# Performance work log

Hardware: AMD Instinct MI355X
Metric: run time of the kernel (lower is better)

## Reference

```python
import jax, jax.numpy as jnp
import numpy as np

D = 1024  # model dimension

def _linear_params(key, d_in, d_out):
    kw, kb = jax.random.split(key)
    bound = 1.0 / np.sqrt(d_in)
    W = jax.random.uniform(kw, (d_out, d_in), minval=-bound, maxval=bound, dtype=jnp.float32)
    b = jax.random.uniform(kb, (d_out,), minval=-bound, maxval=bound, dtype=jnp.float32)
    return W, b

def setup_inputs() -> dict:
    key = jax.random.key(0)
    kx, ki, kq, kk, kv, ko = jax.random.split(key, 6)
    B, S = 4, 2048
    X = jax.random.normal(kx, (B, S, D), dtype=jnp.float32)
    intensity = jax.random.uniform(ki, (B, S, S), dtype=jnp.float32)
    Wq, bq = _linear_params(kq, D, D)
    Wk, bk = _linear_params(kk, D, D)
    Wv, bv = _linear_params(kv, D, D)
    Wo, bo = _linear_params(ko, D, D)
    return {"X": X, "intensity": intensity,
            "Wq": Wq, "bq": bq, "Wk": Wk, "bk": bk,
            "Wv": Wv, "bv": bv, "Wo": Wo, "bo": bo}

def reference(X, intensity, Wq, bq, Wk, bk, Wv, bv, Wo, bo):
    d_k = Wq.shape[0]
    q = X @ Wq.T + bq                      # [B,S,D]
    k = X @ Wk.T + bk                      # [B,S,D]
    v = X @ Wv.T + bv                      # [B,S,D]
    scores = jnp.einsum('bsd,btd->bst', q, k) / jnp.sqrt(jnp.asarray(d_k, X.dtype))
    attn = jax.nn.softmax(scores, axis=-1) + intensity  # non-standard additive epilogue
    out = jnp.einsum('bst,btd->bsd', attn, v)
    return out @ Wo.T + bo
```

## Files before the change

kernel.cpp:

```cpp
#include <hip/hip_runtime.h>

typedef __attribute__((ext_vector_type(8))) short bf16x8;
typedef __attribute__((ext_vector_type(4))) float f32x4;

#define LDS_TILE (48 * 1024)
#define NBUF 3
#define LDS_TOTAL (NBUF * LDS_TILE)

__device__ __forceinline__ unsigned short f2bf(float f) {
  union { float f; unsigned u; } a; a.f = f;
  unsigned u = a.u;
  unsigned r = (u + 0x7FFFu + ((u >> 16) & 1u)) >> 16;
  return (unsigned short)r;
}

__device__ __forceinline__ void stage16(const void* g, void* l) {
  __builtin_amdgcn_global_load_lds((const __attribute__((address_space(1))) unsigned int*)g,
                                   (__attribute__((address_space(3))) unsigned int*)l,
                                   16, 0, 0);
}

template<bool OUT_BF16, int BIAS_MODE>
__global__ __launch_bounds__(512) void gemm_nt(
    const unsigned short* __restrict__ A,
    const unsigned short* __restrict__ B,
    void* __restrict__ Cv,
    const float* __restrict__ bias,
    float scale, int K,
    int lda, int ldb, int ldc,
    long batchA, long batchB, long batchC)
{
  extern __shared__ char smem[];

  const int gx = gridDim.x, gy = gridDim.y;
  int bid = blockIdx.x + gx * (blockIdx.y + gy * blockIdx.z);
  const int nwg = gx * gy * gridDim.z;
  const int q = nwg >> 3;
  int wg = (bid & 7) * q + (bid >> 3);
  const int tx = wg % gx;
  int rest = wg / gx;
  const int ty = rest % gy;
  const int tz = rest / gy;

  const int tid  = threadIdx.x;
  const int lane = tid & 63;
  const int wid  = tid >> 6;
  const int wm   = wid & 3;
  const int wn   = wid >> 2;

  A += (long)tz * batchA;
  B += (long)tz * batchB;
  const int tileM = tx * 256;
  const int tileN = ty * 128;

  const int srow = tid >> 3;
  const int scol = (((tid & 7) ^ (srow & 7)) << 3);
  const unsigned short* ga[4];
  const unsigned short* gb[2];
#pragma unroll
  for (int j = 0; j < 4; ++j) ga[j] = A + (size_t)(tileM + j * 64 + srow) * lda + scol;
#pragma unroll
  for (int j = 0; j < 2; ++j) gb[j] = B + (size_t)(tileN + j * 64 + srow) * ldb + scol;

  const int frow  = lane & 15;
  const int k0slot = (lane >> 4) ^ (lane & 7);
  const int aoff = (wm * 64 + frow) * 128;
  const int boff = 32768 + (wn * 64 + frow) * 128;

  f32x4 acc[4][4];
#pragma unroll
  for (int m = 0; m < 4; ++m)
#pragma unroll
    for (int n = 0; n < 4; ++n) acc[m][n] = (f32x4){0.f, 0.f, 0.f, 0.f};

  const int nt = K >> 6;

#define STAGE(t)                                                         \
  do {                                                                   \
    char* d_ = smem + ((t) % NBUF) * LDS_TILE;                           \
    const int kc_ = (t) << 6;                                            \
    _Pragma("unroll")                                                    \
    for (int j = 0; j < 4; ++j) stage16(ga[j] + kc_, d_ + j * 8192 + tid * 16); \
    _Pragma("unroll")                                                    \
    for (int j = 0; j < 2; ++j) stage16(gb[j] + kc_, d_ + 32768 + j * 8192 + tid * 16); \
  } while (0)

#define COMPUTE(t)                                                       \
  do {                                                                   \
    const char* d_ = smem + ((t) % NBUF) * LDS_TILE;                     \
    bf16x8 af[4][2], bfr[4][2];                                          \
    _Pragma("unroll")                                                    \
    for (int ks = 0; ks < 2; ++ks) {                                     \
      const int so_ = ((k0slot ^ (ks << 2)) << 4);                       \
      _Pragma("unroll")                                                  \
      for (int m = 0; m < 4; ++m)                                        \
        af[m][ks] = *(const bf16x8*)(d_ + aoff + m * 2048 + so_);        \
      _Pragma("unroll")                                                  \
      for (int n = 0; n < 4; ++n)                                        \
        bfr[n][ks] = *(const bf16x8*)(d_ + boff + n * 2048 + so_);       \
    }                                                                    \
    __builtin_amdgcn_s_setprio(1);                                       \
    _Pragma("unroll")                                                    \
    for (int ks = 0; ks < 2; ++ks)                                       \
      _Pragma("unroll")                                                  \
      for (int m = 0; m < 4; ++m)                                        \
        _Pragma("unroll")                                                \
        for (int n = 0; n < 4; ++n)                                      \
          acc[m][n] = __builtin_amdgcn_mfma_f32_16x16x32_bf16(af[m][ks], bfr[n][ks], acc[m][n], 0, 0, 0); \
    __builtin_amdgcn_s_setprio(0);                                       \
  } while (0)

  STAGE(0);
  STAGE(1);
  asm volatile("s_waitcnt vmcnt(6)" ::: "memory");
  __builtin_amdgcn_s_barrier();

  for (int t = 0; t < nt - 2; ++t) {
    STAGE(t + 2);
    COMPUTE(t);
    asm volatile("s_waitcnt vmcnt(6)" ::: "memory");
    __builtin_amdgcn_s_barrier();
  }
  COMPUTE(nt - 2);
  asm volatile("s_waitcnt vmcnt(0)" ::: "memory");
  __builtin_amdgcn_s_barrier();
  COMPUTE(nt - 1);

#undef STAGE
#undef COMPUTE

  const int ro = (lane >> 4) << 2;
  const int co = lane & 15;
#pragma unroll
  for (int m = 0; m < 4; ++m) {
#pragma unroll
    for (int n = 0; n < 4; ++n) {
      const int row0 = tileM + wm * 64 + m * 16 + ro;
      const int col  = tileN + wn * 64 + n * 16 + co;
#pragma unroll
      for (int r = 0; r < 4; ++r) {
        float v = acc[m][n][r] * scale;
        const int row = row0 + r;
        if (BIAS_MODE == 1) v += bias[col];
        if (BIAS_MODE == 2) v += bias[row];
        const size_t ci = (size_t)(tz * batchC) + (size_t)row * ldc + col;
        if (OUT_BF16) ((unsigned short*)Cv)[ci] = f2bf(v);
        else          ((float*)Cv)[ci] = v;
      }
    }
  }
}

__global__ __launch_bounds__(256) void softmax_add_bf16(
    float* __restrict__ scores, const float* __restrict__ inten)
{
  const int row = blockIdx.x;
  float* srow = scores + (size_t)row * 2048;
  const float* irow = inten + (size_t)row * 2048;
  const int t = threadIdx.x;
  const int lane = t & 63, wid = t >> 6;

  float v[8];
  float mx = -3.4e38f;
#pragma unroll
  for (int j = 0; j < 8; ++j) { v[j] = srow[t + j * 256]; mx = fmaxf(mx, v[j]); }

  __shared__ float red[8];
#pragma unroll
  for (int o = 32; o; o >>= 1) mx = fmaxf(mx, __shfl_xor(mx, o));
  if (lane == 0) red[wid] = mx;
  __syncthreads();
  mx = fmaxf(fmaxf(red[0], red[1]), fmaxf(red[2], red[3]));

  float s = 0.f;
#pragma unroll
  for (int j = 0; j < 8; ++j) { v[j] = __expf(v[j] - mx); s += v[j]; }
#pragma unroll
  for (int o = 32; o; o >>= 1) s += __shfl_xor(s, o);
  if (lane == 0) red[4 + wid] = s;
  __syncthreads();
  s = red[4] + red[5] + red[6] + red[7];
  const float inv = 1.f / s;

  unsigned short* arow = (unsigned short*)srow;
#pragma unroll
  for (int j = 0; j < 8; ++j)
    arow[t + j * 256] = f2bf(v[j] * inv + irow[t + j * 256]);
}

__global__ __launch_bounds__(256) void cvt_bf16(
    const float* __restrict__ in, unsigned short* __restrict__ out, int n)
{
  const int i = (blockIdx.x * 256 + threadIdx.x) * 4;
  if (i >= n) return;
  const float4 f = *(const float4*)(in + i);
  ushort4 o;
  o.x = f2bf(f.x); o.y = f2bf(f.y); o.z = f2bf(f.z); o.w = f2bf(f.w);
  *(ushort4*)(out + i) = o;
}

extern "C" void kernel_launch(void* const* d_in, const int* in_sizes, int n_in,
                              void* d_out, int out_size, void* d_ws, size_t ws_size,
                              hipStream_t stream)
{
  const float* X     = (const float*)d_in[0];
  const float* inten = (const float*)d_in[1];
  const float* Wq = (const float*)d_in[2];
  const float* bq = (const float*)d_in[3];
  const float* Wk = (const float*)d_in[4];
  const float* bk = (const float*)d_in[5];
  const float* Wv = (const float*)d_in[6];
  const float* bv = (const float*)d_in[7];
  const float* Wo = (const float*)d_in[8];
  const float* bo = (const float*)d_in[9];
  float* out = (float*)d_out;

  const int B = 4, S = 2048, D = 1024;
  const int MS = B * S;
  char* ws = (char*)d_ws;
  const size_t MB = 1 << 20;
  unsigned short* Xb  = (unsigned short*)(ws);
  unsigned short* Wqb = (unsigned short*)(ws + 16 * MB);
  unsigned short* Wkb = (unsigned short*)(ws + 18 * MB);
  unsigned short* Wvb = (unsigned short*)(ws + 20 * MB);
  unsigned short* Wob = (unsigned short*)(ws + 22 * MB);
  unsigned short* Q   = (unsigned short*)(ws + 24 * MB);
  unsigned short* Kb  = (unsigned short*)(ws + 40 * MB);
  unsigned short* Vt  = (unsigned short*)(ws + 56 * MB);
  unsigned short* Oa  = (unsigned short*)(ws + 72 * MB);
  float*          Sc  = (float*)(ws + 88 * MB);

  hipFuncSetAttribute((const void*)gemm_nt<true, 1>,  hipFuncAttributeMaxDynamicSharedMemorySize, LDS_TOTAL);
  hipFuncSetAttribute((const void*)gemm_nt<true, 2>,  hipFuncAttributeMaxDynamicSharedMemorySize, LDS_TOTAL);
  hipFuncSetAttribute((const void*)gemm_nt<false, 0>, hipFuncAttributeMaxDynamicSharedMemorySize, LDS_TOTAL);
  hipFuncSetAttribute((const void*)gemm_nt<true, 0>,  hipFuncAttributeMaxDynamicSharedMemorySize, LDS_TOTAL);
  hipFuncSetAttribute((const void*)gemm_nt<false, 1>, hipFuncAttributeMaxDynamicSharedMemorySize, LDS_TOTAL);

  cvt_bf16<<<(MS * D) / 1024, 256, 0, stream>>>(X,  Xb,  MS * D);
  cvt_bf16<<<(D * D) / 1024, 256, 0, stream>>>(Wq, Wqb, D * D);
  cvt_bf16<<<(D * D) / 1024, 256, 0, stream>>>(Wk, Wkb, D * D);
  cvt_bf16<<<(D * D) / 1024, 256, 0, stream>>>(Wv, Wvb, D * D);
  cvt_bf16<<<(D * D) / 1024, 256, 0, stream>>>(Wo, Wob, D * D);

  dim3 gproj(MS / 256, D / 128, 1);
  gemm_nt<true, 1><<<gproj, 512, LDS_TOTAL, stream>>>(Xb, Wqb, Q,  bq, 1.f, D, D, D, D, 0, 0, 0);
  gemm_nt<true, 1><<<gproj, 512, LDS_TOTAL, stream>>>(Xb, Wkb, Kb, bk, 1.f, D, D, D, D, 0, 0, 0);

  dim3 gvt(D / 256, S / 128, B);
  gemm_nt<true, 2><<<gvt, 512, LDS_TOTAL, stream>>>(Wvb, Xb, Vt, bv, 1.f, D, D, D, S,
                                                    0, (long)S * D, (long)D * S);

  dim3 gsc(S / 256, S / 128, B);
  gemm_nt<false, 0><<<gsc, 512, LDS_TOTAL, stream>>>(Q, Kb, Sc, nullptr, 0.03125f, D,
                                                     D, D, S,
                                                     (long)S * D, (long)S * D, (long)S * S);

  softmax_add_bf16<<<B * S, 256, 0, stream>>>(Sc, inten);

  dim3 gav(S / 256, D / 128, B);
  gemm_nt<true, 0><<<gav, 512, LDS_TOTAL, stream>>>((unsigned short*)Sc, Vt, Oa, nullptr,
                                                    1.f, S, 2 * S, S, D,
                                                    (long)S * 2 * S, (long)D * S, (long)S * D);

  gemm_nt<false, 1><<<gproj, 512, LDS_TOTAL, stream>>>(Oa, Wob, out, bo, 1.f, D, D, D, D, 0, 0, 0);
}
```

Measured before the change: 349.8 us.

## Enlarge GEMM tiles to 256x256 with K=32 four-stage pipeline and batch Q/K projections

The GEMM kernel moves from 256x128 tiles with K-step 64 and three LDS buffers to 256x256 tiles with K-step 32 and four 32KB buffers. Each warp now computes 128x64 with 8x4 MFMA accumulators and uses a new swizzle for the narrower rows. The Q and K projections are merged into a single launch via the z dimension, with a second bias pointer picked by tz parity. The goal is more reuse per loaded byte and fewer launches, at the cost of doubled accumulator registers, a launch_bounds occupancy hint that may cause spills, and fewer workgroups per GEMM.

```diff
diff --git a/kernel.cpp b/kernel.cpp
--- a/kernel.cpp
+++ b/kernel.cpp
@@ -3,8 +3,8 @@
 typedef __attribute__((ext_vector_type(8))) short bf16x8;
 typedef __attribute__((ext_vector_type(4))) float f32x4;
 
-#define LDS_TILE (48 * 1024)
-#define NBUF 3
+#define LDS_TILE 32768
+#define NBUF 4
 #define LDS_TOTAL (NBUF * LDS_TILE)
 
 __device__ __forceinline__ unsigned short f2bf(float f) {
@@ -21,11 +21,12 @@
 }
 
 template<bool OUT_BF16, int BIAS_MODE>
-__global__ __launch_bounds__(512) void gemm_nt(
+__global__ __launch_bounds__(512, 2) void gemm_nt(
     const unsigned short* __restrict__ A,
     const unsigned short* __restrict__ B,
     void* __restrict__ Cv,
     const float* __restrict__ bias,
+    const float* __restrict__ bias2,
     float scale, int K,
     int lda, int ldb, int ldc,
     long batchA, long batchB, long batchC)
@@ -45,82 +46,80 @@
   const int tid  = threadIdx.x;
   const int lane = tid & 63;
   const int wid  = tid >> 6;
-  const int wm   = wid & 3;
-  const int wn   = wid >> 2;
+  const int wm   = wid >> 2;
+  const int wn   = wid & 3;
 
   A += (long)tz * batchA;
   B += (long)tz * batchB;
   const int tileM = tx * 256;
-  const int tileN = ty * 128;
-
-  const int srow = tid >> 3;
-  const int scol = (((tid & 7) ^ (srow & 7)) << 3);
-  const unsigned short* ga[4];
+  const int tileN = ty * 256;
+
+  const int srow = tid >> 2;
+  const int fs   = ((srow & 3) ^ ((srow >> 2) & 1));
+  const int scol = (((tid & 3) ^ fs) << 3);
+  const unsigned short* ga[2];
   const unsigned short* gb[2];
 #pragma unroll
-  for (int j = 0; j < 4; ++j) ga[j] = A + (size_t)(tileM + j * 64 + srow) * lda + scol;
-#pragma unroll
-  for (int j = 0; j < 2; ++j) gb[j] = B + (size_t)(tileN + j * 64 + srow) * ldb + scol;
-
-  const int frow  = lane & 15;
-  const int k0slot = (lane >> 4) ^ (lane & 7);
-  const int aoff = (wm * 64 + frow) * 128;
-  const int boff = 32768 + (wn * 64 + frow) * 128;
-
-  f32x4 acc[4][4];
-#pragma unroll
-  for (int m = 0; m < 4; ++m)
+  for (int g = 0; g < 2; ++g) ga[g] = A + (size_t)(tileM + g * 128 + srow) * lda + scol;
+#pragma unroll
+  for (int g = 0; g < 2; ++g) gb[g] = B + (size_t)(tileN + g * 128 + srow) * ldb + scol;
+
+  const int fl   = lane & 15;
+  const int fr   = ((fl & 3) ^ ((fl >> 2) & 1));
+  const int swz16 = (((lane >> 4) ^ fr) << 4);
+  const int paoff = (wm * 128 + fl) * 64 + swz16;
+  const int pboff = 16384 + (wn * 64 + fl) * 64 + swz16;
+
+  f32x4 acc[8][4];
+#pragma unroll
+  for (int m = 0; m < 8; ++m)
 #pragma unroll
     for (int n = 0; n < 4; ++n) acc[m][n] = (f32x4){0.f, 0.f, 0.f, 0.f};
 
-  const int nt = K >> 6;
-
-#define STAGE(t)                                                         \
-  do {                                                                   \
-    char* d_ = smem + ((t) % NBUF) * LDS_TILE;                           \
-    const int kc_ = (t) << 6;                                            \
-    _Pragma("unroll")                                                    \
-    for (int j = 0; j < 4; ++j) stage16(ga[j] + kc_, d_ + j * 8192 + tid * 16); \
-    _Pragma("unroll")                                                    \
-    for (int j = 0; j < 2; ++j) stage16(gb[j] + kc_, d_ + 32768 + j * 8192 + tid * 16); \
+  const int nt = K >> 5;
+
+#define STAGE(t)                                                            \
+  do {                                                                      \
+    char* d_ = smem + ((t) & 3) * LDS_TILE;                                 \
+    const int kc_ = (t) << 5;                                               \
+    _Pragma("unroll")                                                       \
+    for (int g = 0; g < 2; ++g) stage16(ga[g] + kc_, d_ + g * 8192 + tid * 16); \
+    _Pragma("unroll")                                                       \
+    for (int g = 0; g < 2; ++g) stage16(gb[g] + kc_, d_ + 16384 + g * 8192 + tid * 16); \
   } while (0)
 
-#define COMPUTE(t)                                                       \
-  do {                                                                   \
-    const char* d_ = smem + ((t) % NBUF) * LDS_TILE;                     \
-    bf16x8 af[4][2], bfr[4][2];                                          \
-    _Pragma("unroll")                                                    \
-    for (int ks = 0; ks < 2; ++ks) {                                     \
-      const int so_ = ((k0slot ^ (ks << 2)) << 4);                       \
-      _Pragma("unroll")                                                  \
-      for (int m = 0; m < 4; ++m)                                        \
-        af[m][ks] = *(const bf16x8*)(d_ + aoff + m * 2048 + so_);        \
-      _Pragma("unroll")                                                  \
-      for (int n = 0; n < 4; ++n)                                        \
-        bfr[n][ks] = *(const bf16x8*)(d_ + boff + n * 2048 + so_);       \
-    }                                                                    \
-    __builtin_amdgcn_s_setprio(1);                                       \
-    _Pragma("unroll")                                                    \
-    for (int ks = 0; ks < 2; ++ks)                                       \
-      _Pragma("unroll")                                                  \
-      for (int m = 0; m < 4; ++m)                                        \
-        _Pragma("unroll")                                                \
-        for (int n = 0; n < 4; ++n)                                      \
-          acc[m][n] = __builtin_amdgcn_mfma_f32_16x16x32_bf16(af[m][ks], bfr[n][ks], acc[m][n], 0, 0, 0); \
-    __builtin_amdgcn_s_setprio(0);                                       \
+#define COMPUTE(t)                                                          \
+  do {                                                                      \
+    const char* d_ = smem + ((t) & 3) * LDS_TILE;                           \
+    bf16x8 af[8], bfv[4];                                                   \
+    _Pragma("unroll")                                                       \
+    for (int m = 0; m < 8; ++m) af[m]  = *(const bf16x8*)(d_ + paoff + m * 1024); \
+    _Pragma("unroll")                                                       \
+    for (int n = 0; n < 4; ++n) bfv[n] = *(const bf16x8*)(d_ + pboff + n * 1024); \
+    __builtin_amdgcn_s_setprio(1);                                          \
+    _Pragma("unroll")                                                       \
+    for (int m = 0; m < 8; ++m)                                             \
+      _Pragma("unroll")                                                     \
+      for (int n = 0; n < 4; ++n)                                           \
+        acc[m][n] = __builtin_amdgcn_mfma_f32_16x16x32_bf16(af[m], bfv[n], acc[m][n], 0, 0, 0); \
+    __builtin_amdgcn_s_setprio(0);                                          \
   } while (0)
 
   STAGE(0);
   STAGE(1);
-  asm volatile("s_waitcnt vmcnt(6)" ::: "memory");
+  STAGE(2);
+  asm volatile("s_waitcnt vmcnt(8)" ::: "memory");
   __builtin_amdgcn_s_barrier();
 
-  for (int t = 0; t < nt - 2; ++t) {
-    STAGE(t + 2);
+  for (int t = 0; t < nt - 3; ++t) {
+    STAGE(t + 3);
     COMPUTE(t);
-    asm volatile("s_waitcnt vmcnt(6)" ::: "memory");
+    asm volatile("s_waitcnt vmcnt(8)" ::: "memory");
     __builtin_amdgcn_s_barrier();
   }
+  COMPUTE(nt - 3);
+  asm volatile("s_waitcnt vmcnt(4)" ::: "memory");
+  __builtin_amdgcn_s_barrier();
   COMPUTE(nt - 2);
   asm volatile("s_waitcnt vmcnt(0)" ::: "memory");
   __builtin_amdgcn_s_barrier();
@@ -129,20 +128,21 @@
 #undef STAGE
 #undef COMPUTE
 
+  const float* bptr = (tz & 1) ? bias2 : bias;
   const int ro = (lane >> 4) << 2;
   const int co = lane & 15;
 #pragma unroll
-  for (int m = 0; m < 4; ++m) {
+  for (int m = 0; m < 8; ++m) {
 #pragma unroll
     for (int n = 0; n < 4; ++n) {
-      const int row0 = tileM + wm * 64 + m * 16 + ro;
+      const int row0 = tileM + wm * 128 + m * 16 + ro;
       const int col  = tileN + wn * 64 + n * 16 + co;
 #pragma unroll
       for (int r = 0; r < 4; ++r) {
         float v = acc[m][n][r] * scale;
         const int row = row0 + r;
-        if (BIAS_MODE == 1) v += bias[col];
-        if (BIAS_MODE == 2) v += bias[row];
+        if (BIAS_MODE == 1) v += bptr[col];
+        if (BIAS_MODE == 2) v += bptr[row];
         const size_t ci = (size_t)(tz * batchC) + (size_t)row * ldc + col;
         if (OUT_BF16) ((unsigned short*)Cv)[ci] = f2bf(v);
         else          ((float*)Cv)[ci] = v;
@@ -242,25 +242,29 @@
   cvt_bf16<<<(D * D) / 1024, 256, 0, stream>>>(Wv, Wvb, D * D);
   cvt_bf16<<<(D * D) / 1024, 256, 0, stream>>>(Wo, Wob, D * D);
 
-  dim3 gproj(MS / 256, D / 128, 1);
-  gemm_nt<true, 1><<<gproj, 512, LDS_TOTAL, stream>>>(Xb, Wqb, Q,  bq, 1.f, D, D, D, D, 0, 0, 0);
-  gemm_nt<true, 1><<<gproj, 512, LDS_TOTAL, stream>>>(Xb, Wkb, Kb, bk, 1.f, D, D, D, D, 0, 0, 0);
-
-  dim3 gvt(D / 256, S / 128, B);
-  gemm_nt<true, 2><<<gvt, 512, LDS_TOTAL, stream>>>(Wvb, Xb, Vt, bv, 1.f, D, D, D, S,
-                                                    0, (long)S * D, (long)D * S);
-
-  dim3 gsc(S / 256, S / 128, B);
-  gemm_nt<false, 0><<<gsc, 512, LDS_TOTAL, stream>>>(Q, Kb, Sc, nullptr, 0.03125f, D,
-                                                     D, D, S,
-                                                     (long)S * D, (long)S * D, (long)S * S);
+  dim3 gqk(MS / 256, D / 256, 2);
+  gemm_nt<true, 1><<<gqk, 512, LDS_TOTAL, stream>>>(
+      Xb, Wqb, Q, bq, bk, 1.f, D, D, D, D,
+      0, (long)(Wkb - Wqb), (long)(Kb - Q));
+
+  dim3 gvt(D / 256, S / 256, B);
+  gemm_nt<true, 2><<<gvt, 512, LDS_TOTAL, stream>>>(
+      Wvb, Xb, Vt, bv, bv, 1.f, D, D, D, S,
+      0, (long)S * D, (long)D * S);
+
+  dim3 gsc(S / 256, S / 256, B);
+  gemm_nt<false, 0><<<gsc, 512, LDS_TOTAL, stream>>>(
+      Q, Kb, Sc, nullptr, nullptr, 0.03125f, D, D, D, S,
+      (long)S * D, (long)S * D, (long)S * S);
 
   softmax_add_bf16<<<B * S, 256, 0, stream>>>(Sc, inten);
 
-  dim3 gav(S / 256, D / 128, B);
-  gemm_nt<true, 0><<<gav, 512, LDS_TOTAL, stream>>>((unsigned short*)Sc, Vt, Oa, nullptr,
-                                                    1.f, S, 2 * S, S, D,
-                                                    (long)S * 2 * S, (long)D * S, (long)S * D);
-
-  gemm_nt<false, 1><<<gproj, 512, LDS_TOTAL, stream>>>(Oa, Wob, out, bo, 1.f, D, D, D, D, 0, 0, 0);
-}
+  dim3 gav(S / 256, D / 256, B);
+  gemm_nt<true, 0><<<gav, 512, LDS_TOTAL, stream>>>(
+      (unsigned short*)Sc, Vt, Oa, nullptr, nullptr, 1.f, S, 2 * S, S, D,
+      (long)S * 2 * S, (long)D * S, (long)S * D);
+
+  dim3 gout(MS / 256, D / 256, 1);
+  gemm_nt<false, 1><<<gout, 512, LDS_TOTAL, stream>>>(
+      Oa, Wob, out, bo, bo, 1.f, D, D, D, D, 0, 0, 0);
+}
```

Measured after the change: 376.9 us. 7.7% more time.

## Store scores in bf16, vectorize softmax, merge weight casts and Q/K projections

Applied to the files above, without the earlier changes.

The score GEMM now writes bf16 instead of fp32, halving the score write and the softmax read. The softmax moves to contiguous 8-element vector loads and stores and writes to a separate dense attention buffer, so the AV GEMM reads a tight stride. The four weight conversions merge into one launch, and the Q and K projections run as a single batched GEMM with per-batch bias selection. Scores are rounded to bf16 before softmax, which loses some precision.

```diff
diff --git a/kernel.cpp b/kernel.cpp
--- a/kernel.cpp
+++ b/kernel.cpp
@@ -12,6 +12,11 @@
   unsigned u = a.u;
   unsigned r = (u + 0x7FFFu + ((u >> 16) & 1u)) >> 16;
   return (unsigned short)r;
+}
+
+__device__ __forceinline__ float bf2f(unsigned short s) {
+  union { unsigned u; float f; } c; c.u = ((unsigned)s) << 16;
+  return c.f;
 }
 
 __device__ __forceinline__ void stage16(const void* g, void* l) {
@@ -26,6 +31,7 @@
     const unsigned short* __restrict__ B,
     void* __restrict__ Cv,
     const float* __restrict__ bias,
+    const float* __restrict__ bias2,
     float scale, int K,
     int lda, int ldb, int ldc,
     long batchA, long batchB, long batchC)
@@ -129,6 +135,7 @@
 #undef STAGE
 #undef COMPUTE
 
+  const float* bptr = (tz & 1) ? bias2 : bias;
   const int ro = (lane >> 4) << 2;
   const int co = lane & 15;
 #pragma unroll
@@ -141,8 +148,8 @@
       for (int r = 0; r < 4; ++r) {
         float v = acc[m][n][r] * scale;
         const int row = row0 + r;
-        if (BIAS_MODE == 1) v += bias[col];
-        if (BIAS_MODE == 2) v += bias[row];
+        if (BIAS_MODE == 1) v += bptr[col];
+        if (BIAS_MODE == 2) v += bptr[row];
         const size_t ci = (size_t)(tz * batchC) + (size_t)row * ldc + col;
         if (OUT_BF16) ((unsigned short*)Cv)[ci] = f2bf(v);
         else          ((float*)Cv)[ci] = v;
@@ -152,18 +159,25 @@
 }
 
 __global__ __launch_bounds__(256) void softmax_add_bf16(
-    float* __restrict__ scores, const float* __restrict__ inten)
+    const unsigned short* __restrict__ scores,
+    const float* __restrict__ inten,
+    unsigned short* __restrict__ attn)
 {
   const int row = blockIdx.x;
-  float* srow = scores + (size_t)row * 2048;
+  const unsigned short* srow = scores + (size_t)row * 2048;
   const float* irow = inten + (size_t)row * 2048;
+  unsigned short* arow = attn + (size_t)row * 2048;
   const int t = threadIdx.x;
   const int lane = t & 63, wid = t >> 6;
 
+  const bf16x8 raw = *(const bf16x8*)(srow + t * 8);
   float v[8];
   float mx = -3.4e38f;
 #pragma unroll
-  for (int j = 0; j < 8; ++j) { v[j] = srow[t + j * 256]; mx = fmaxf(mx, v[j]); }
+  for (int j = 0; j < 8; ++j) {
+    v[j] = bf2f((unsigned short)raw[j]);
+    mx = fmaxf(mx, v[j]);
+  }
 
   __shared__ float red[8];
 #pragma unroll
@@ -182,10 +196,13 @@
   s = red[4] + red[5] + red[6] + red[7];
   const float inv = 1.f / s;
 
-  unsigned short* arow = (unsigned short*)srow;
-#pragma unroll
-  for (int j = 0; j < 8; ++j)
-    arow[t + j * 256] = f2bf(v[j] * inv + irow[t + j * 256]);
+  const float4 i0 = *(const float4*)(irow + t * 8);
+  const float4 i1 = *(const float4*)(irow + t * 8 + 4);
+  const float ia[8] = {i0.x, i0.y, i0.z, i0.w, i1.x, i1.y, i1.z, i1.w};
+  bf16x8 o;
+#pragma unroll
+  for (int j = 0; j < 8; ++j) o[j] = (short)f2bf(v[j] * inv + ia[j]);
+  *(bf16x8*)(arow + t * 8) = o;
 }
 
 __global__ __launch_bounds__(256) void cvt_bf16(
@@ -197,6 +214,21 @@
   ushort4 o;
   o.x = f2bf(f.x); o.y = f2bf(f.y); o.z = f2bf(f.z); o.w = f2bf(f.w);
   *(ushort4*)(out + i) = o;
+}
+
+__global__ __launch_bounds__(256) void cvt_w4(
+    const float* __restrict__ w0, const float* __restrict__ w1,
+    const float* __restrict__ w2, const float* __restrict__ w3,
+    unsigned short* __restrict__ out)
+{
+  const int b = blockIdx.x;
+  const int w = b >> 10;
+  const float* src = (w == 0) ? w0 : (w == 1) ? w1 : (w == 2) ? w2 : w3;
+  const int local = ((b & 1023) * 256 + threadIdx.x) * 4;
+  const float4 f = *(const float4*)(src + local);
+  ushort4 o;
+  o.x = f2bf(f.x); o.y = f2bf(f.y); o.z = f2bf(f.z); o.w = f2bf(f.w);
+  *(ushort4*)(out + (size_t)w * 1048576 + local) = o;
 }
 
 extern "C" void kernel_launch(void* const* d_in, const int* in_sizes, int n_in,
@@ -228,39 +260,40 @@
   unsigned short* Kb  = (unsigned short*)(ws + 40 * MB);
   unsigned short* Vt  = (unsigned short*)(ws + 56 * MB);
   unsigned short* Oa  = (unsigned short*)(ws + 72 * MB);
-  float*          Sc  = (float*)(ws + 88 * MB);
+  unsigned short* Sc  = (unsigned short*)(ws + 88 * MB);
+  unsigned short* At  = (unsigned short*)(ws + 120 * MB);
 
   hipFuncSetAttribute((const void*)gemm_nt<true, 1>,  hipFuncAttributeMaxDynamicSharedMemorySize, LDS_TOTAL);
   hipFuncSetAttribute((const void*)gemm_nt<true, 2>,  hipFuncAttributeMaxDynamicSharedMemorySize, LDS_TOTAL);
-  hipFuncSetAttribute((const void*)gemm_nt<false, 0>, hipFuncAttributeMaxDynamicSharedMemorySize, LDS_TOTAL);
   hipFuncSetAttribute((const void*)gemm_nt<true, 0>,  hipFuncAttributeMaxDynamicSharedMemorySize, LDS_TOTAL);
   hipFuncSetAttribute((const void*)gemm_nt<false, 1>, hipFuncAttributeMaxDynamicSharedMemorySize, LDS_TOTAL);
 
-  cvt_bf16<<<(MS * D) / 1024, 256, 0, stream>>>(X,  Xb,  MS * D);
-  cvt_bf16<<<(D * D) / 1024, 256, 0, stream>>>(Wq, Wqb, D * D);
-  cvt_bf16<<<(D * D) / 1024, 256, 0, stream>>>(Wk, Wkb, D * D);
-  cvt_bf16<<<(D * D) / 1024, 256, 0, stream>>>(Wv, Wvb, D * D);
-  cvt_bf16<<<(D * D) / 1024, 256, 0, stream>>>(Wo, Wob, D * D);
-
-  dim3 gproj(MS / 256, D / 128, 1);
-  gemm_nt<true, 1><<<gproj, 512, LDS_TOTAL, stream>>>(Xb, Wqb, Q,  bq, 1.f, D, D, D, D, 0, 0, 0);
-  gemm_nt<true, 1><<<gproj, 512, LDS_TOTAL, stream>>>(Xb, Wkb, Kb, bk, 1.f, D, D, D, D, 0, 0, 0);
+  cvt_bf16<<<(MS * D) / 1024, 256, 0, stream>>>(X, Xb, MS * D);
+  cvt_w4<<<4096, 256, 0, stream>>>(Wq, Wk, Wv, Wo, Wqb);
+
+  dim3 gqk(MS / 256, D / 128, 2);
+  gemm_nt<true, 1><<<gqk, 512, LDS_TOTAL, stream>>>(
+      Xb, Wqb, Q, bq, bk, 1.f, D, D, D, D,
+      0, (long)(Wkb - Wqb), (long)(Kb - Q));
 
   dim3 gvt(D / 256, S / 128, B);
-  gemm_nt<true, 2><<<gvt, 512, LDS_TOTAL, stream>>>(Wvb, Xb, Vt, bv, 1.f, D, D, D, S,
-                                                    0, (long)S * D, (long)D * S);
+  gemm_nt<true, 2><<<gvt, 512, LDS_TOTAL, stream>>>(
+      Wvb, Xb, Vt, bv, bv, 1.f, D, D, D, S,
+      0, (long)S * D, (long)D * S);
 
   dim3 gsc(S / 256, S / 128, B);
-  gemm_nt<false, 0><<<gsc, 512, LDS_TOTAL, stream>>>(Q, Kb, Sc, nullptr, 0.03125f, D,
-                                                     D, D, S,
-                                                     (long)S * D, (long)S * D, (long)S * S);
-
-  softmax_add_bf16<<<B * S, 256, 0, stream>>>(Sc, inten);
+  gemm_nt<true, 0><<<gsc, 512, LDS_TOTAL, stream>>>(
+      Q, Kb, Sc, nullptr, nullptr, 0.03125f, D, D, D, S,
+      (long)S * D, (long)S * D, (long)S * S);
+
+  softmax_add_bf16<<<B * S, 256, 0, stream>>>(Sc, inten, At);
 
   dim3 gav(S / 256, D / 128, B);
-  gemm_nt<true, 0><<<gav, 512, LDS_TOTAL, stream>>>((unsigned short*)Sc, Vt, Oa, nullptr,
-                                                    1.f, S, 2 * S, S, D,
-                                                    (long)S * 2 * S, (long)D * S, (long)S * D);
-
-  gemm_nt<false, 1><<<gproj, 512, LDS_TOTAL, stream>>>(Oa, Wob, out, bo, 1.f, D, D, D, D, 0, 0, 0);
-}
+  gemm_nt<true, 0><<<gav, 512, LDS_TOTAL, stream>>>(
+      At, Vt, Oa, nullptr, nullptr, 1.f, S, S, S, D,
+      (long)S * S, (long)D * S, (long)S * D);
+
+  dim3 gout(MS / 256, D / 128, 1);
+  gemm_nt<false, 1><<<gout, 512, LDS_TOTAL, stream>>>(
+      Oa, Wob, out, bo, bo, 1.f, D, D, D, D, 0, 0, 0);
+}
```

New measurement: 344.2 us. About the same (-1.6%).
